# Kernel optimization log

Measured on AMD Instinct MI355X. Metric: run time of the kernel, lower is better.

The kernel has to match this reference:

```python
import jax, jax.numpy as jnp
import numpy as np
from jax import lax

# Quantization / conv config (mirrors QuantizedConv2d init args)
INPUT_ZP = -3
OUTPUT_ZP = 5
INPUT_SCALE = 0.05
OUTPUT_SCALE = 0.1
STRIDE = 1
PAD = (1, 1)   # (pad_h, pad_w)
DILATION = 1
GROUPS = 1
FEATURE_BITWIDTH = 8
QMIN = -(1 << (FEATURE_BITWIDTH - 1))          # -128
QMAX = (1 << (FEATURE_BITWIDTH - 1)) - 1       # 127

N, CIN, H, W = 32, 128, 56, 56
COUT, KH, KW = 256, 3, 3


def setup_inputs() -> dict:
    key = jax.random.key(0)
    k1, k2, k3, k4 = jax.random.split(key, 4)
    # int8-range quantized input / weight (stored as int32 arrays)
    x = jax.random.randint(k1, (N, CIN, H, W), 0, 256, dtype=jnp.int32) - 128
    weight = jax.random.randint(k2, (COUT, CIN, KH, KW), 0, 128, dtype=jnp.int32) - 64
    bias = jax.random.randint(k3, (COUT,), -32, 32, dtype=jnp.int32)
    # per-output-channel weight scale, shape [COUT,1,1] so it broadcasts over NCHW
    weight_scale = jax.random.uniform(k4, (COUT, 1, 1), dtype=jnp.float32) * 0.01 + 1e-4
    return {"x": x, "weight": weight, "bias": bias, "weight_scale": weight_scale}


def reference(x, weight, bias, weight_scale):
    ph, pw = PAD
    # Pad with the input zero point (quantized-domain padding)
    x_f = jnp.pad(x.astype(jnp.float32), ((0, 0), (0, 0), (ph, ph), (pw, pw)),
                  constant_values=float(INPUT_ZP))
    w_f = weight.astype(jnp.float32)
    b_f = bias.astype(jnp.float32)[None, :, None, None]
    # float32 conv (GPU path of the original), padding already applied
    acc = lax.conv_general_dilated(
        x_f, w_f,
        window_strides=(STRIDE, STRIDE),
        padding='VALID',
        rhs_dilation=(DILATION, DILATION),
        feature_group_count=GROUPS,
        dimension_numbers=('NCHW', 'OIHW', 'NCHW'))
    # original: conv2d(..., bias=q_bias) then round -> int32, then bias added AGAIN
    out = jnp.round(acc + b_f).astype(jnp.int32)
    out = out + bias[None, :, None, None]
    # dequant -> requant epilogue with per-channel weight scale
    out = (out.astype(jnp.float32) * INPUT_SCALE * weight_scale[None]
           / OUTPUT_SCALE + OUTPUT_ZP)
    out = jnp.clip(jnp.round(out), QMIN, QMAX).astype(jnp.int8)
    return out
```

## Files before the change

### kernel.cpp

```cpp
#include <hip/hip_runtime.h>


typedef __attribute__((ext_vector_type(4))) int i32x4;

#define NB_N 32
#define CIN 128
#define HH 56
#define WW 56
#define PH 58
#define COUT 256
#define PIX_PER_IMG (HH*WW)
#define X_IMG_INTS (PIX_PER_IMG*CIN)
#define XP_ROW_BYTES (PH*CIN)
#define XP_IMG_BYTES (PH*XP_ROW_BYTES)
#define XQ_PAD_BYTES ((size_t)NB_N*XP_IMG_BYTES)
#define A_BYTES (6*XP_ROW_BYTES)

__global__ __launch_bounds__(256) void halo_kernel(signed char* __restrict__ xq) {
    const i32x4 pad = {(int)0xFDFDFDFD, (int)0xFDFDFDFD, (int)0xFDFDFDFD, (int)0xFDFDFDFD};
    signed char* img = xq + (size_t)blockIdx.x * XP_IMG_BYTES;
    for (int t = threadIdx.x; t < 928; t += 256) {
        int r = (t < 464) ? 0 : 57;
        int off = ((t < 464) ? t : t - 464) * 16;
        *(i32x4*)(img + (size_t)r * XP_ROW_BYTES + off) = pad;
    }
    for (int t = threadIdx.x; t < 896; t += 256) {
        int px = t >> 3;
        int q = t & 7;
        int r = 1 + (px >> 1);
        int w = (px & 1) ? 57 : 0;
        *(i32x4*)(img + ((size_t)r * PH + w) * CIN + q * 16) = pad;
    }
}

#define TS 132
__global__ __launch_bounds__(256) void pack_x_kernel(const int* __restrict__ x,
                                                     signed char* __restrict__ xq) {
    __shared__ signed char tile[WW * TS];
    int nh = blockIdx.x;
    int n = nh / HH, h = nh - n * HH;
    const int* src = x + (size_t)n * X_IMG_INTS + h * WW;
    for (int i = 0; i < 7; ++i) {
        int idx = i * 256 + threadIdx.x;
        int c = idx / 14;
        int q = idx - c * 14;
        i32x4 v = *(const i32x4*)(src + c * PIX_PER_IMG + q * 4);
#pragma unroll
        for (int k = 0; k < 4; ++k)
            tile[(q * 4 + k) * TS + c] = (signed char)v[k];
    }
    __syncthreads();
    int* dst = (int*)(xq + (size_t)n * XP_IMG_BYTES + ((size_t)(h + 1) * PH + 1) * CIN);
    for (int i = 0; i < 7; ++i) {
        int t = i * 256 + threadIdx.x;
        int w = t >> 5, c4 = t & 31;
        dst[w * 32 + c4] = *(const int*)(tile + w * TS + c4 * 4);
    }
}

__global__ __launch_bounds__(256) void pack_w_kernel(const int* __restrict__ w,
                                                     signed char* __restrict__ wq) {
    int idx = blockIdx.x * 256 + threadIdx.x;
    if (idx >= 9 * 2 * 16 * 64) return;
    int lane = idx & 63;
    int fid = idx >> 6;
    int t = fid / 32;
    int rem = fid - t * 32;
    int kb = rem >> 4;
    int nf = rem & 15;
    int cout = nf * 16 + (lane & 15);
    int cinb = kb * 64 + (lane >> 4) * 16;
    int kh = t / 3, kw = t - kh * 3;
    union { signed char b[16]; i32x4 v; } u;
#pragma unroll
    for (int j = 0; j < 16; ++j) {
        int cin = cinb + j;
        u.b[j] = (signed char)w[((cout * CIN + cin) * 3 + kh) * 3 + kw];
    }
    *(i32x4*)(wq + (size_t)idx * 16) = u.v;
}

__global__ __launch_bounds__(256, 2) void conv_kernel(const signed char* __restrict__ xq,
                                                      const signed char* __restrict__ wq,
                                                      const int* __restrict__ bias,
                                                      const float* __restrict__ wscale,
                                                      int* __restrict__ out) {
    __shared__ __align__(16) signed char lds[A_BYTES];
    const int tid = threadIdx.x;
    const int lane = tid & 63, wv = tid >> 6;
    const int row = lane & 15, grp = lane >> 4;

    int orig = (blockIdx.x & 7) * 112 + (blockIdx.x >> 3);
    int n = orig / 28;
    int rr = orig - n * 28;
    int rb = rr >> 1;
    int cb = rr & 1;
    int pxhalf = wv >> 1, chalf = wv & 1;

    const signed char* ximg = xq + (size_t)n * XP_IMG_BYTES + (size_t)rb * 4 * XP_ROW_BYTES;

#pragma unroll
    for (int k = 0; k < 11; ++k) {
        int d = k * 4096 + tid * 16;
        if (d < A_BYTES) {
            int g = d ^ (((d >> 7) & 7) << 4);
            i32x4 v = *(const i32x4*)(ximg + g);
            *(i32x4*)(lds + d) = v;
        }
    }
    __syncthreads();

    int pc[7];
#pragma unroll
    for (int m = 0; m < 7; ++m) {
        int off = pxhalf * 112 + m * 16 + row;
        int lr = (off >= 56) + (off >= 112) + (off >= 168);
        int w = off - lr * 56;
        pc[m] = (lr + 1) * PH + (w + 1);
    }

    const int tapd[9] = {-PH - 1, -PH, -PH + 1, -1, 0, 1, PH - 1, PH, PH + 1};

    const signed char* wbase = wq + (size_t)(cb * 8 + chalf * 4) * 1024 + lane * 16;

    i32x4 acc[7][4] = {};
    i32x4 bn[4];
#pragma unroll
    for (int j = 0; j < 4; ++j) bn[j] = *(const i32x4*)(wbase + j * 1024);

#pragma unroll
    for (int s = 0; s < 18; ++s) {
        const int t = s >> 1, kb = s & 1;
        i32x4 b[4];
#pragma unroll
        for (int j = 0; j < 4; ++j) b[j] = bn[j];
        if (s < 17) {
#pragma unroll
            for (int j = 0; j < 4; ++j)
                bn[j] = *(const i32x4*)(wbase + (s + 1) * 16384 + j * 1024);
        }
        i32x4 a[7];
#pragma unroll
        for (int m = 0; m < 7; ++m) {
            int pix = pc[m] + tapd[t];
            int g = (pix << 7) + (kb << 6) + (grp << 4);
            int d = g ^ ((pix & 7) << 4);
            a[m] = *(const i32x4*)(lds + d);
        }
#pragma unroll
        for (int m = 0; m < 7; ++m)
#pragma unroll
            for (int j = 0; j < 4; ++j)
                acc[m][j] = __builtin_amdgcn_mfma_i32_16x16x64_i8(a[m], b[j], acc[m][j], 0, 0, 0);
    }

    float sc[4];
    int b2[4];
    const int coutbase = cb * 128 + chalf * 64;
#pragma unroll
    for (int j = 0; j < 4; ++j) {
        int cout = coutbase + j * 16 + row;
        sc[j] = wscale[cout] * 0.5f;
        b2[j] = 2 * bias[cout];
    }
    const int pixbase = rb * 224 + pxhalf * 112;
#pragma unroll
    for (int m = 0; m < 7; ++m) {
        int pl = pixbase + m * 16 + grp * 4;
        size_t obase = (size_t)n * (COUT * PIX_PER_IMG) + pl;
#pragma unroll
        for (int j = 0; j < 4; ++j) {
            int cout = coutbase + j * 16 + row;
            i32x4 v;
#pragma unroll
            for (int r = 0; r < 4; ++r) {
                int o = acc[m][j][r] + b2[j];
                float f = fmaf((float)o, sc[j], 5.0f);
                f = rintf(f);
                f = fminf(fmaxf(f, -128.0f), 127.0f);
                v[r] = (int)f;
            }
            *(i32x4*)(out + obase + (size_t)cout * PIX_PER_IMG) = v;
        }
    }
}

extern "C" void kernel_launch(void* const* d_in, const int* in_sizes, int n_in,
                              void* d_out, int out_size, void* d_ws, size_t ws_size,
                              hipStream_t stream) {
    const int* x = (const int*)d_in[0];
    const int* w = (const int*)d_in[1];
    const int* bias = (const int*)d_in[2];
    const float* ws = (const float*)d_in[3];
    int* out = (int*)d_out;

    signed char* xq = (signed char*)d_ws;
    signed char* wq = xq + XQ_PAD_BYTES;

    halo_kernel<<<NB_N, 256, 0, stream>>>(xq);
    pack_x_kernel<<<NB_N * HH, 256, 0, stream>>>(x, xq);
    pack_w_kernel<<<72, 256, 0, stream>>>(w, wq);
    conv_kernel<<<896, 256, 0, stream>>>(xq, wq, bias, ws, out);
}
```

Before: 69.77 us.

## Pack input channels into int words in LDS, raise conv occupancy, prioritize MFMA

The input-packing kernel now loads four channel rows per thread and packs their low bytes into one 32-bit word. It writes whole words into a padded int LDS tile instead of making scattered single-byte stores. Separately, the conv kernel's launch bound asks for 3 blocks per SIMD instead of 2, and s_setprio raises wave priority around the MFMA block. The packing change cuts LDS byte-store traffic. The occupancy hint may force register spilling of the 112-register accumulator array, which could hurt the main kernel.

```diff
diff --git a/kernel.cpp b/kernel.cpp
--- a/kernel.cpp
+++ b/kernel.cpp
@@ -33,28 +33,38 @@
     }
 }
 
-#define TS 132
+#define WPR 33
 __global__ __launch_bounds__(256) void pack_x_kernel(const int* __restrict__ x,
                                                      signed char* __restrict__ xq) {
-    __shared__ signed char tile[WW * TS];
+    __shared__ int tile[WW * WPR];
     int nh = blockIdx.x;
     int n = nh / HH, h = nh - n * HH;
     const int* src = x + (size_t)n * X_IMG_INTS + h * WW;
-    for (int i = 0; i < 7; ++i) {
-        int idx = i * 256 + threadIdx.x;
-        int c = idx / 14;
-        int q = idx - c * 14;
-        i32x4 v = *(const i32x4*)(src + c * PIX_PER_IMG + q * 4);
-#pragma unroll
-        for (int k = 0; k < 4; ++k)
-            tile[(q * 4 + k) * TS + c] = (signed char)v[k];
+    int q = threadIdx.x & 15;
+    int cg4 = threadIdx.x >> 4;
+    if (q < 14) {
+#pragma unroll
+        for (int i = 0; i < 2; ++i) {
+            int cg = cg4 + i * 16;
+            i32x4 v0 = *(const i32x4*)(src + (cg * 4 + 0) * PIX_PER_IMG + q * 4);
+            i32x4 v1 = *(const i32x4*)(src + (cg * 4 + 1) * PIX_PER_IMG + q * 4);
+            i32x4 v2 = *(const i32x4*)(src + (cg * 4 + 2) * PIX_PER_IMG + q * 4);
+            i32x4 v3 = *(const i32x4*)(src + (cg * 4 + 3) * PIX_PER_IMG + q * 4);
+#pragma unroll
+            for (int j = 0; j < 4; ++j) {
+                int word = (v0[j] & 255) | ((v1[j] & 255) << 8) |
+                           ((v2[j] & 255) << 16) | (v3[j] << 24);
+                tile[(q * 4 + j) * WPR + cg] = word;
+            }
+        }
     }
     __syncthreads();
     int* dst = (int*)(xq + (size_t)n * XP_IMG_BYTES + ((size_t)(h + 1) * PH + 1) * CIN);
+#pragma unroll
     for (int i = 0; i < 7; ++i) {
         int t = i * 256 + threadIdx.x;
         int w = t >> 5, c4 = t & 31;
-        dst[w * 32 + c4] = *(const int*)(tile + w * TS + c4 * 4);
+        dst[w * 32 + c4] = tile[w * WPR + c4];
     }
 }
 
@@ -80,7 +90,7 @@
     *(i32x4*)(wq + (size_t)idx * 16) = u.v;
 }
 
-__global__ __launch_bounds__(256, 2) void conv_kernel(const signed char* __restrict__ xq,
+__global__ __launch_bounds__(256, 3) void conv_kernel(const signed char* __restrict__ xq,
                                                       const signed char* __restrict__ wq,
                                                       const int* __restrict__ bias,
                                                       const float* __restrict__ wscale,
@@ -147,11 +157,13 @@
             int d = g ^ ((pix & 7) << 4);
             a[m] = *(const i32x4*)(lds + d);
         }
+        __builtin_amdgcn_s_setprio(1);
 #pragma unroll
         for (int m = 0; m < 7; ++m)
 #pragma unroll
             for (int j = 0; j < 4; ++j)
                 acc[m][j] = __builtin_amdgcn_mfma_i32_16x16x64_i8(a[m], b[j], acc[m][j], 0, 0, 0);
+        __builtin_amdgcn_s_setprio(0);
     }
 
     float sc[4];
```

Result: slower. 171.5 us (+145.7%).
